# Kernel tuning notes

Measured on AMD Instinct MI355X. Metric: run time of the kernel, lower is better.

The kernel has to match this reference:

```python
import jax, jax.numpy as jnp
import numpy as np

DIM = 8          # per-head dim
ATT_EPS = 1e-15  # LiteMLA eps
BN_EPS = 1e-5    # torch BatchNorm2d default eps


def conv2d(x, w, groups=1, pad=0):
    # x: NCHW, w: OIHW
    return jax.lax.conv_general_dilated(
        x, w, window_strides=(1, 1), padding=[(pad, pad), (pad, pad)],
        dimension_numbers=('NCHW', 'OIHW', 'NCHW'), feature_group_count=groups)


def setup_inputs() -> dict:
    key = jax.random.key(0)
    ks = jax.random.split(key, 6)
    B, C, H, W = 4, 128, 128, 128
    heads = C // DIM            # 16
    t3 = 3 * C                  # 3*total_dim = 384
    x = jax.random.normal(ks[0], (B, C, H, W), jnp.float32)
    w_qkv = jax.random.normal(ks[1], (t3, C, 1, 1), jnp.float32) * 0.02
    w_dw = jax.random.normal(ks[2], (t3, 1, 5, 5), jnp.float32) * 0.02      # depthwise 5x5
    w_pw = jax.random.normal(ks[3], (t3, t3 // (3 * heads), 1, 1), jnp.float32) * 0.05  # grouped 1x1, groups=3*heads
    w_proj = jax.random.normal(ks[4], (C, 2 * C, 1, 1), jnp.float32) * 0.02  # proj 1x1: 2C -> C
    bn_gamma = jnp.ones((C,), jnp.float32)
    bn_beta = jnp.zeros((C,), jnp.float32)
    bn_mean = jnp.zeros((C,), jnp.float32)
    bn_var = jnp.ones((C,), jnp.float32)
    return dict(x=x, w_qkv=w_qkv, w_dw=w_dw, w_pw=w_pw, w_proj=w_proj,
                bn_gamma=bn_gamma, bn_beta=bn_beta, bn_mean=bn_mean, bn_var=bn_var)


def reference(x, w_qkv, w_dw, w_pw, w_proj, bn_gamma, bn_beta, bn_mean, bn_var):
    # qkv: 1x1 conv, no norm / no act
    qkv = conv2d(x, w_qkv)                                  # (B, 3C, H, W)
    t3 = w_qkv.shape[0]
    # aggreg[0]: depthwise 5x5 + grouped 1x1
    groups_pw = t3 // w_pw.shape[1]                         # 3*heads
    agg = conv2d(conv2d(qkv, w_dw, groups=t3, pad=2), w_pw, groups=groups_pw)
    qkv = jnp.concatenate([qkv, agg], axis=1)               # (B, 6C, H, W)

    B, _, H, W = qkv.shape
    N = H * W
    qkv = qkv.reshape(B, -1, 3 * DIM, N)                    # (B, 2*heads, 3*dim, N)
    q = jax.nn.relu(qkv[:, :, :DIM])                        # (B, h, d, N)
    k = jax.nn.relu(qkv[:, :, DIM:2 * DIM])                 # (B, h, d, N)
    v = qkv[:, :, 2 * DIM:]                                 # (B, h, d, N)
    # pad v with a row of ones for normalization
    v = jnp.concatenate([v, jnp.ones_like(v[:, :, :1])], axis=2)  # (B, h, d+1, N)

    vk = jnp.einsum('bhdn,bhen->bhde', v, k)                # (B, h, d+1, d)
    out = jnp.einsum('bhde,bhen->bhdn', vk, q)              # (B, h, d+1, N)
    out = out[:, :, :-1] / (out[:, :, -1:] + ATT_EPS)       # (B, h, d, N)
    out = out.reshape(B, -1, H, W)                          # (B, 2C, H, W)

    # proj: 1x1 conv + BatchNorm2d (inference), no act
    out = conv2d(out, w_proj)                               # (B, C, H, W)
    inv = bn_gamma / jnp.sqrt(bn_var + BN_EPS)
    out = out * inv[:, None, None] + (bn_beta - bn_mean * inv)[:, None, None]
    return out
```

## Files before the change

### kernel.cpp

```cpp
#include <hip/hip_runtime.h>

#define BB 4
#define CIN 128
#define T3 384
#define HH 128
#define WW 128
#define NPIX 16384
#define QKV_ELE (BB*T3*NPIX)

#define SEC 4160
#define KGP 1040
#define PLN 520

typedef __attribute__((ext_vector_type(8))) short bf16x8;
typedef __attribute__((ext_vector_type(4))) float f32x4;

__device__ __forceinline__ unsigned splitpack(float x) {
  unsigned u = __float_as_uint(x);
  unsigned hb = (u + 0x7fffu + ((u >> 16) & 1u)) >> 16;
  float lo = x - __uint_as_float(hb << 16);
  unsigned ul = __float_as_uint(lo);
  unsigned lb = (ul + 0x7fffu + ((ul >> 16) & 1u)) >> 16;
  return (hb << 16) | (lb & 0xffffu);
}

__device__ __forceinline__ void packpair(float a, float b, unsigned& hi, unsigned& lo) {
  unsigned p0 = splitpack(a), p1 = splitpack(b);
  hi = (p1 & 0xffff0000u) | (p0 >> 16);
  lo = (p1 << 16) | (p0 & 0xffffu);
}

__global__ __launch_bounds__(256) void k0_wprep(const float* __restrict__ wqkv,
                                                unsigned* __restrict__ wimg,
                                                float* __restrict__ zbuf) {
  int id = blockIdx.x * 256 + threadIdx.x;
  if (id < 16) zbuf[id] = 0.f;
  int i = id & 3;
  int co = (id >> 2) & 127;
  int kgrp = (id >> 9) & 3;
  int c = (id >> 11) & 3;
  int m = id >> 13;
  int ci = c * 32 + kgrp * 8 + 2 * i;
  const float* wrow = wqkv + (size_t)(m * 128 + co) * 128 + ci;
  unsigned hi, lo;
  packpair(wrow[0], wrow[1], hi, lo);
  size_t base = (size_t)(m * 4 + c) * SEC + kgrp * KGP + co * 4 + i;
  wimg[base] = hi;
  wimg[base + PLN] = lo;
}

__global__ __launch_bounds__(256) void k1_qkv_mfma(const float* __restrict__ x,
                                                   const unsigned* __restrict__ wimg,
                                                   float* __restrict__ qkv) {
  __shared__ __align__(16) unsigned Xp[4 * KGP];
  __shared__ __align__(16) unsigned Wp[4 * KGP];
  const int t = threadIdx.x;
  const int p = blockIdx.x;
  const int qd = p / 24;
  const int r_ = p - qd * 24;
  const int m = r_ >> 3;
  const int tt = qd * 8 + (r_ & 7);
  const int n0 = (tt & 127) * 128;
  const int b = tt >> 7;
  const float* xb = x + (size_t)b * CIN * NPIX + n0;

  const int l = t & 63;
  const int w = t >> 6;
  const int g = l >> 4;
  const int lc = l & 15;
  const int ch = w >> 1;
  const int nh = w & 1;
  const int kg = t >> 6;
  const int nn_ = t & 63;

  f32x4 acc[4][4];
  #pragma unroll
  for (int i = 0; i < 4; ++i)
    #pragma unroll
    for (int j = 0; j < 4; ++j) acc[i][j] = (f32x4){0.f, 0.f, 0.f, 0.f};

  for (int c = 0; c < 4; ++c) {
    {
      const uint4* wsrc = (const uint4*)(wimg + (size_t)(m * 4 + c) * SEC);
      uint4* wdst = (uint4*)Wp;
      #pragma unroll
      for (int r = 0; r < 5; ++r) {
        int idx = t + r * 256;
        if (idx < 1040) wdst[idx] = wsrc[idx];
      }
    }
    {
      const float* colbase = xb + (size_t)(c * 32 + kg * 8) * NPIX;
      #pragma unroll
      for (int half = 0; half < 2; ++half) {
        int n = nn_ + half * 64;
        const float* colp = colbase + n;
        unsigned hp[4], lp[4];
        #pragma unroll
        for (int i = 0; i < 4; ++i)
          packpair(colp[(size_t)(2 * i) * NPIX], colp[(size_t)(2 * i + 1) * NPIX],
                   hp[i], lp[i]);
        *(uint4*)&Xp[kg * KGP + n * 4] = make_uint4(hp[0], hp[1], hp[2], hp[3]);
        *(uint4*)&Xp[kg * KGP + PLN + n * 4] = make_uint4(lp[0], lp[1], lp[2], lp[3]);
      }
    }
    __syncthreads();

    bf16x8 bh[4], bl[4];
    #pragma unroll
    for (int ng = 0; ng < 4; ++ng) {
      const int nb = (nh * 64 + ng * 16 + lc) * 4;
      bh[ng] = *(const bf16x8*)&Xp[g * KGP + nb];
      bl[ng] = *(const bf16x8*)&Xp[g * KGP + PLN + nb];
    }
    #pragma unroll
    for (int cg = 0; cg < 4; ++cg) {
      const int cb = (ch * 64 + cg * 16 + lc) * 4;
      bf16x8 ah = *(const bf16x8*)&Wp[g * KGP + cb];
      bf16x8 al = *(const bf16x8*)&Wp[g * KGP + PLN + cb];
      #pragma unroll
      for (int ng = 0; ng < 4; ++ng) {
        acc[cg][ng] = __builtin_amdgcn_mfma_f32_16x16x32_bf16(ah, bh[ng], acc[cg][ng], 0, 0, 0);
        acc[cg][ng] = __builtin_amdgcn_mfma_f32_16x16x32_bf16(ah, bl[ng], acc[cg][ng], 0, 0, 0);
        acc[cg][ng] = __builtin_amdgcn_mfma_f32_16x16x32_bf16(al, bh[ng], acc[cg][ng], 0, 0, 0);
      }
    }
    __syncthreads();
  }
  #pragma unroll
  for (int cg = 0; cg < 4; ++cg) {
    const size_t corow = (size_t)b * T3 + m * 128 + ch * 64 + cg * 16 + g * 4;
    #pragma unroll
    for (int ng = 0; ng < 4; ++ng) {
      const int nn = n0 + nh * 64 + ng * 16 + lc;
      #pragma unroll
      for (int rr = 0; rr < 4; ++rr)
        qkv[(corow + rr) * NPIX + nn] = acc[cg][ng][rr];
    }
  }
}

#define PDW 36

__device__ __forceinline__ void dw_compute(const float* __restrict__ plane,
                                           const float* __restrict__ w25,
                                           const float* __restrict__ zbuf,
                                           int x0, int y0, int xq, int yg,
                                           float dacc[4][4]) {
  const int gx0 = x0 + 4 * xq - 4;
  const bool ex0 = (gx0 >= 0);
  const bool ex2 = (gx0 + 11 < WW);
  f32x4 u[8][3];
  #pragma unroll
  for (int r = 0; r < 8; ++r) {
    const int gy = y0 + 4 * yg - 2 + r;
    const bool iny = (unsigned)gy < (unsigned)HH;
    const float* rp = plane + gy * WW + gx0;
    const float* p0 = (iny && ex0) ? rp : zbuf;
    const float* p1 = iny ? (rp + 4) : zbuf;
    const float* p2 = (iny && ex2) ? (rp + 8) : zbuf;
    u[r][0] = *(const f32x4*)p0;
    u[r][1] = *(const f32x4*)p1;
    u[r][2] = *(const f32x4*)p2;
  }
  #pragma unroll
  for (int jy = 0; jy < 4; ++jy)
    #pragma unroll
    for (int jx = 0; jx < 4; ++jx) dacc[jy][jx] = 0.f;
  #pragma unroll
  for (int r = 0; r < 8; ++r) {
    float vals[12] = {u[r][0][0], u[r][0][1], u[r][0][2], u[r][0][3],
                      u[r][1][0], u[r][1][1], u[r][1][2], u[r][1][3],
                      u[r][2][0], u[r][2][1], u[r][2][2], u[r][2][3]};
    #pragma unroll
    for (int jy = 0; jy < 4; ++jy) {
      int ky = r - jy;
      if (ky < 0 || ky > 4) continue;
      #pragma unroll
      for (int kx = 0; kx < 5; ++kx) {
        float wv = w25[ky * 5 + kx];
        #pragma unroll
        for (int jx = 0; jx < 4; ++jx)
          dacc[jy][jx] += wv * vals[jx + kx + 2];
      }
    }
  }
}

__device__ __forceinline__ void vk_reduce(const float* __restrict__ kb,
                                          const float* __restrict__ vb,
                                          float* __restrict__ pr, int t) {
  const int wv = t >> 6;
  const int lane = t & 63;
  const int d0 = wv * 2;
  float accA[8], accB[8], accS[8];
  #pragma unroll
  for (int e = 0; e < 8; ++e) { accA[e] = 0.f; accB[e] = 0.f; accS[e] = 0.f; }
  #pragma unroll
  for (int it = 0; it < 8; ++it) {
    int p = it * 64 + lane;
    float kv[8];
    #pragma unroll
    for (int e = 0; e < 8; ++e) kv[e] = kb[e * 512 + p];
    float vA = vb[d0 * 512 + p];
    float vB = vb[(d0 + 1) * 512 + p];
    #pragma unroll
    for (int e = 0; e < 8; ++e) { accA[e] += vA * kv[e]; accB[e] += vB * kv[e]; }
    if (wv == 0) {
      #pragma unroll
      for (int e = 0; e < 8; ++e) accS[e] += kv[e];
    }
  }
  #pragma unroll
  for (int e = 0; e < 8; ++e) {
    #pragma unroll
    for (int m = 1; m < 64; m <<= 1) {
      accA[e] += __shfl_xor(accA[e], m);
      accB[e] += __shfl_xor(accB[e], m);
    }
  }
  if (wv == 0) {
    #pragma unroll
    for (int e = 0; e < 8; ++e)
      #pragma unroll
      for (int m = 1; m < 64; m <<= 1) accS[e] += __shfl_xor(accS[e], m);
  }
  if (lane == 0) {
    #pragma unroll
    for (int e = 0; e < 8; ++e) {
      pr[d0 * 8 + e] = accA[e];
      pr[(d0 + 1) * 8 + e] = accB[e];
    }
    if (wv == 0) {
      #pragma unroll
      for (int e = 0; e < 8; ++e) pr[64 + e] = accS[e];
    }
  }
}

__global__ __launch_bounds__(256, 4) void k2_fused(const float* __restrict__ qkv,
                                                   const float* __restrict__ wdw,
                                                   const float* __restrict__ wpw,
                                                   const float* __restrict__ zbuf,
                                                   float* __restrict__ agg,
                                                   float* __restrict__ part2) {
  __shared__ __align__(16) float bufA[8 * 16 * PDW];
  __shared__ __align__(16) float bufB[8 * 16 * PDW];
  __shared__ float wds[24][25];
  __shared__ float wps[192];
  const int t = threadIdx.x;
  const int p = blockIdx.x;
  const int L = (p & 7) * 256 + (p >> 3);
  const int z = L >> 5;
  const int rem = L & 31;
  const int x0 = (rem & 3) * 32;
  const int y0 = (rem >> 2) * 16;
  const int b = z >> 4;
  const int hh = z & 15;
  const float* src = qkv + ((size_t)b * T3 + hh * 24) * NPIX;

  for (int idx = t; idx < 600; idx += 256)
    wds[idx / 25][idx % 25] = wdw[(size_t)hh * 600 + idx];
  if (t < 192) wps[t] = wpw[hh * 192 + t];
  __syncthreads();

  const int ch = t >> 5;
  const int xq = t & 7;
  const int yg = (t >> 3) & 3;

  {
    float daccK[4][4], daccV[4][4];
    dw_compute(src + (size_t)(8 + ch) * NPIX, &wds[8 + ch][0], zbuf, x0, y0, xq, yg, daccK);
    dw_compute(src + (size_t)(16 + ch) * NPIX, &wds[16 + ch][0], zbuf, x0, y0, xq, yg, daccV);
    #pragma unroll
    for (int jy = 0; jy < 4; ++jy) {
      *(float4*)&bufA[ch * (16 * PDW) + (yg * 4 + jy) * PDW + xq * 4] =
          make_float4(daccK[jy][0], daccK[jy][1], daccK[jy][2], daccK[jy][3]);
      *(float4*)&bufB[ch * (16 * PDW) + (yg * 4 + jy) * PDW + xq * 4] =
          make_float4(daccV[jy][0], daccV[jy][1], daccV[jy][2], daccV[jy][3]);
    }
  }
  __syncthreads();

  float kout[2][8], vout[2][8];
  #pragma unroll
  for (int pp = 0; pp < 2; ++pp) {
    int pix = t + pp * 256;
    int py = pix >> 5, px = pix & 31;
    float dvA[8], dvB[8];
    #pragma unroll
    for (int ic = 0; ic < 8; ++ic) {
      dvA[ic] = bufA[ic * (16 * PDW) + py * PDW + px];
      dvB[ic] = bufB[ic * (16 * PDW) + py * PDW + px];
    }
    #pragma unroll
    for (int oc = 0; oc < 8; ++oc) {
      float sk = 0.f, sv = 0.f;
      #pragma unroll
      for (int ic = 0; ic < 8; ++ic) {
        sk += wps[64 + oc * 8 + ic] * dvA[ic];
        sv += wps[128 + oc * 8 + ic] * dvB[ic];
      }
      kout[pp][oc] = sk;
      vout[pp][oc] = sv;
    }
  }
  __syncthreads();

  #pragma unroll
  for (int pp = 0; pp < 2; ++pp) {
    int pix = t + pp * 256;
    #pragma unroll
    for (int oc = 0; oc < 8; ++oc) {
      bufA[oc * 512 + pix] = fmaxf(kout[pp][oc], 0.f);
      bufB[oc * 512 + pix] = vout[pp][oc];
    }
  }
  __syncthreads();

  f32x4 rs[8];
  #pragma unroll
  for (int j = 0; j < 8; ++j) {
    int qd2 = t + j * 256;
    int buf = qd2 >> 10;
    int ch2 = (qd2 >> 7) & 7;
    int r2 = qd2 & 127;
    int py = r2 >> 3, qx = r2 & 7;
    const float* gp = src + (size_t)(8 + buf * 8 + ch2) * NPIX + (y0 + py) * WW + x0 + qx * 4;
    rs[j] = *(const f32x4*)gp;
  }
  vk_reduce(bufA, bufB, part2 + ((size_t)(z * 2 + 1) * 32 + rem) * 72, t);
  __syncthreads();

  #pragma unroll
  for (int j = 0; j < 8; ++j) {
    int qd2 = t + j * 256;
    int buf = qd2 >> 10;
    int ch2 = (qd2 >> 7) & 7;
    int r2 = qd2 & 127;
    int py = r2 >> 3, qx = r2 & 7;
    f32x4 v = rs[j];
    if (buf == 0) {
      v[0] = fmaxf(v[0], 0.f); v[1] = fmaxf(v[1], 0.f);
      v[2] = fmaxf(v[2], 0.f); v[3] = fmaxf(v[3], 0.f);
      *(f32x4*)&bufA[ch2 * 512 + py * 32 + qx * 4] = v;
    } else {
      *(f32x4*)&bufB[ch2 * 512 + py * 32 + qx * 4] = v;
    }
  }
  __syncthreads();

  vk_reduce(bufA, bufB, part2 + ((size_t)(z * 2 + 0) * 32 + rem) * 72, t);
  __syncthreads();

  {
    float dacc[4][4];
    dw_compute(src + (size_t)ch * NPIX, &wds[ch][0], zbuf, x0, y0, xq, yg, dacc);
    #pragma unroll
    for (int jy = 0; jy < 4; ++jy)
      *(float4*)&bufA[ch * (16 * PDW) + (yg * 4 + jy) * PDW + xq * 4] =
          make_float4(dacc[jy][0], dacc[jy][1], dacc[jy][2], dacc[jy][3]);
  }
  __syncthreads();
  float* dst = agg + ((size_t)b * T3 + hh * 24) * NPIX + (size_t)y0 * WW + x0;
  #pragma unroll
  for (int pp = 0; pp < 2; ++pp) {
    int pix = t + pp * 256;
    int py = pix >> 5, px = pix & 31;
    float dv[8];
    #pragma unroll
    for (int ic = 0; ic < 8; ++ic) dv[ic] = bufA[ic * (16 * PDW) + py * PDW + px];
    #pragma unroll
    for (int oc = 0; oc < 8; ++oc) {
      float s = 0.f;
      #pragma unroll
      for (int ic = 0; ic < 8; ++ic) s += wps[oc * 8 + ic] * dv[ic];
      dst[(size_t)oc * NPIX + py * WW + px] = s;
    }
  }
}

__global__ __launch_bounds__(128) void k3b_sum(const float* __restrict__ part2,
                                               float* __restrict__ vk) {
  const int bh = blockIdx.x;
  const int j = threadIdx.x;
  if (j < 72) {
    int b = bh >> 5, h = bh & 31;
    int z = b * 16 + (h & 15);
    int ph = h >> 4;
    const float* srcp = part2 + ((size_t)(z * 2 + ph) * 32) * 72 + j;
    float s = 0.f;
    #pragma unroll
    for (int c = 0; c < 32; ++c) s += srcp[(size_t)c * 72];
    vk[(size_t)bh * 72 + j] = s;
  }
}

__global__ __launch_bounds__(256) void k3c_M(const float* __restrict__ wproj,
                                             const float* __restrict__ vk,
                                             const float* __restrict__ gamma,
                                             const float* __restrict__ beta,
                                             const float* __restrict__ mean,
                                             const float* __restrict__ var,
                                             unsigned* __restrict__ Mimg,
                                             float* __restrict__ shiftb) {
  int id = blockIdx.x * 256 + threadIdx.x;
  int i = id & 3;
  int co = (id >> 2) & 127;
  int kgrp = (id >> 9) & 3;
  int cidx = (id >> 11) & 7;
  int b = id >> 14;
  int h = cidx * 4 + kgrp;
  float inv = gamma[co] * rsqrtf(var[co] + 1e-5f);
  const float* wrow = wproj + (size_t)co * 256 + h * 8;
  const float* vkc = vk + ((size_t)b * 32 + h) * 72;
  float s0 = 0.f, s1 = 0.f;
  #pragma unroll
  for (int d = 0; d < 8; ++d) {
    float wv = wrow[d];
    s0 += wv * vkc[d * 8 + 2 * i];
    s1 += wv * vkc[d * 8 + 2 * i + 1];
  }
  unsigned hi, lo;
  packpair(inv * s0, inv * s1, hi, lo);
  size_t base = (size_t)(b * 8 + cidx) * SEC + kgrp * KGP + co * 4 + i;
  Mimg[base] = hi;
  Mimg[base + PLN] = lo;
  if (b == 0 && cidx == 0 && kgrp == 0 && i == 0)
    shiftb[co] = beta[co] - mean[co] * inv;
}

__global__ __launch_bounds__(256) void k4_mfma(const float* __restrict__ qkv,
                                               const float* __restrict__ agg,
                                               const float* __restrict__ vk,
                                               const unsigned* __restrict__ Mimg,
                                               const float* __restrict__ shiftb,
                                               float* __restrict__ out) {
  __shared__ __align__(16) unsigned Ap[4 * KGP];
  __shared__ __align__(16) unsigned Bp[4 * KGP];
  const int t = threadIdx.x;
  const int n0 = blockIdx.x * 128;
  const int b = blockIdx.y;

  const int l = t & 63;
  const int w = t >> 6;
  const int g = l >> 4;
  const int lc = l & 15;
  const int ch = w >> 1;
  const int nh = w & 1;
  const int hj = t >> 6;
  const int nn_ = t & 63;

  f32x4 acc[4][4];
  #pragma unroll
  for (int i = 0; i < 4; ++i)
    #pragma unroll
    for (int j = 0; j < 4; ++j) acc[i][j] = (f32x4){0.f, 0.f, 0.f, 0.f};

  for (int cidx = 0; cidx < 8; ++cidx) {
    {
      const uint4* asrc = (const uint4*)(Mimg + (size_t)(b * 8 + cidx) * SEC);
      uint4* adst = (uint4*)Ap;
      #pragma unroll
      for (int r = 0; r < 5; ++r) {
        int idx = t + r * 256;
        if (idx < 1040) adst[idx] = asrc[idx];
      }
    }
    {
      const int h = cidx * 4 + hj;
      const float* srcb = (h < 16 ? qkv : agg) +
                          ((size_t)b * T3 + (h & 15) * 24) * NPIX + n0;
      const float* vkr = vk + ((size_t)b * 32 + h) * 72 + 64;
      float vv[8];
      #pragma unroll
      for (int e = 0; e < 8; ++e) vv[e] = vkr[e];
      #pragma unroll
      for (int half = 0; half < 2; ++half) {
        int n = nn_ + half * 64;
        float q[8];
        float den = 1e-15f;
        #pragma unroll
        for (int e = 0; e < 8; ++e) {
          q[e] = fmaxf(srcb[(size_t)e * NPIX + n], 0.f);
          den += vv[e] * q[e];
        }
        float rd = 1.0f / den;
        unsigned hp[4], lp[4];
        #pragma unroll
        for (int i = 0; i < 4; ++i)
          packpair(q[2 * i] * rd, q[2 * i + 1] * rd, hp[i], lp[i]);
        *(uint4*)&Bp[hj * KGP + n * 4] = make_uint4(hp[0], hp[1], hp[2], hp[3]);
        *(uint4*)&Bp[hj * KGP + PLN + n * 4] = make_uint4(lp[0], lp[1], lp[2], lp[3]);
      }
    }
    __syncthreads();

    bf16x8 bh[4], bl[4];
    #pragma unroll
    for (int ng = 0; ng < 4; ++ng) {
      const int nb = (nh * 64 + ng * 16 + lc) * 4;
      bh[ng] = *(const bf16x8*)&Bp[g * KGP + nb];
      bl[ng] = *(const bf16x8*)&Bp[g * KGP + PLN + nb];
    }
    #pragma unroll
    for (int cg = 0; cg < 4; ++cg) {
      const int cb = (ch * 64 + cg * 16 + lc) * 4;
      bf16x8 ah = *(const bf16x8*)&Ap[g * KGP + cb];
      bf16x8 al = *(const bf16x8*)&Ap[g * KGP + PLN + cb];
      #pragma unroll
      for (int ng = 0; ng < 4; ++ng) {
        acc[cg][ng] = __builtin_amdgcn_mfma_f32_16x16x32_bf16(ah, bh[ng], acc[cg][ng], 0, 0, 0);
        acc[cg][ng] = __builtin_amdgcn_mfma_f32_16x16x32_bf16(ah, bl[ng], acc[cg][ng], 0, 0, 0);
        acc[cg][ng] = __builtin_amdgcn_mfma_f32_16x16x32_bf16(al, bh[ng], acc[cg][ng], 0, 0, 0);
      }
    }
    __syncthreads();
  }
  #pragma unroll
  for (int cg = 0; cg < 4; ++cg) {
    const int cobase = ch * 64 + cg * 16 + g * 4;
    #pragma unroll
    for (int ng = 0; ng < 4; ++ng) {
      const int nn = n0 + nh * 64 + ng * 16 + lc;
      #pragma unroll
      for (int rr = 0; rr < 4; ++rr) {
        int co = cobase + rr;
        out[((size_t)b * 128 + co) * NPIX + nn] = acc[cg][ng][rr] + shiftb[co];
      }
    }
  }
}

__global__ void fill_sentinel(float* o, int n) {
  int i = blockIdx.x * 256 + threadIdx.x;
  if (i < n) o[i] = 12345.0f;
}

extern "C" void kernel_launch(void* const* d_in, const int* in_sizes, int n_in,
                              void* d_out, int out_size, void* d_ws, size_t ws_size,
                              hipStream_t stream) {
  const float* x     = (const float*)d_in[0];
  const float* wqkv  = (const float*)d_in[1];
  const float* wdw   = (const float*)d_in[2];
  const float* wpw   = (const float*)d_in[3];
  const float* wproj = (const float*)d_in[4];
  const float* gamma = (const float*)d_in[5];
  const float* beta  = (const float*)d_in[6];
  const float* mean  = (const float*)d_in[7];
  const float* var   = (const float*)d_in[8];
  float* out = (float*)d_out;
  float* ws = (float*)d_ws;

  const size_t part2F = 64 * 2 * 32 * 72;
  const size_t mimgF = 32 * SEC;
  const size_t wimgF = 12 * SEC;
  const size_t needF = (size_t)QKV_ELE * 2 + part2F + 9216 + 128 + mimgF + wimgF + 16;
  if (ws_size < needF * 4) {
    fill_sentinel<<<dim3((out_size + 255) / 256), dim3(256), 0, stream>>>(out, out_size);
    return;
  }
  float* qkv    = ws;
  float* agg    = qkv + QKV_ELE;
  float* part2  = agg + QKV_ELE;
  float* vkbuf  = part2 + part2F;
  float* shiftb = vkbuf + 9216;
  unsigned* Mimg = (unsigned*)(shiftb + 128);
  unsigned* wimg = Mimg + mimgF;
  float* zbuf   = (float*)(wimg + wimgF);

  k0_wprep<<<dim3(96), 256, 0, stream>>>(wqkv, wimg, zbuf);
  k1_qkv_mfma<<<dim3(1536), 256, 0, stream>>>(x, wimg, qkv);
  k2_fused<<<dim3(2048), 256, 0, stream>>>(qkv, wdw, wpw, zbuf, agg, part2);
  k3b_sum<<<dim3(128), 128, 0, stream>>>(part2, vkbuf);
  k3c_M<<<dim3(256), 256, 0, stream>>>(wproj, vkbuf, gamma, beta, mean, var, Mimg, shiftb);
  k4_mfma<<<dim3(128, 4), 256, 0, stream>>>(qkv, agg, vkbuf, Mimg, shiftb, out);
}
```

Baseline: 160.3 us.

## Split fused depthwise kernel into Q and KV kernels, halve k4 pixel tile

The fused k2 kernel is split in two. k2_q computes the Q-branch depthwise and grouped conv into agg. k2_kv computes the K/V branches with the V loads issued early to overlap the K pointwise stage, then does the vk reductions. Separately, k4 now covers 64 pixels per block instead of 128, doubling its grid to raise occupancy and parallelism. The cost is an extra launch, re-reading of the qkv planes and A-operand loads across more blocks, and higher LDS use in k2_kv.

```diff
diff --git a/kernel.cpp b/kernel.cpp
--- a/kernel.cpp
+++ b/kernel.cpp
@@ -11,6 +11,8 @@
 #define SEC 4160
 #define KGP 1040
 #define PLN 520
+#define KGPB 520
+#define PLNB 260
 
 typedef __attribute__((ext_vector_type(8))) short bf16x8;
 typedef __attribute__((ext_vector_type(4))) float f32x4;
@@ -142,15 +144,13 @@
 
 #define PDW 36
 
-__device__ __forceinline__ void dw_compute(const float* __restrict__ plane,
-                                           const float* __restrict__ w25,
-                                           const float* __restrict__ zbuf,
-                                           int x0, int y0, int xq, int yg,
-                                           float dacc[4][4]) {
+__device__ __forceinline__ void dw_load(const float* __restrict__ plane,
+                                        const float* __restrict__ zbuf,
+                                        int x0, int y0, int xq, int yg,
+                                        f32x4 u[8][3]) {
   const int gx0 = x0 + 4 * xq - 4;
   const bool ex0 = (gx0 >= 0);
   const bool ex2 = (gx0 + 11 < WW);
-  f32x4 u[8][3];
   #pragma unroll
   for (int r = 0; r < 8; ++r) {
     const int gy = y0 + 4 * yg - 2 + r;
@@ -163,6 +163,11 @@
     u[r][1] = *(const f32x4*)p1;
     u[r][2] = *(const f32x4*)p2;
   }
+}
+
+__device__ __forceinline__ void dw_math(const f32x4 u[8][3],
+                                        const float* __restrict__ w25,
+                                        float dacc[4][4]) {
   #pragma unroll
   for (int jy = 0; jy < 4; ++jy)
     #pragma unroll
@@ -187,67 +192,14 @@
   }
 }
 
-__device__ __forceinline__ void vk_reduce(const float* __restrict__ kb,
-                                          const float* __restrict__ vb,
-                                          float* __restrict__ pr, int t) {
-  const int wv = t >> 6;
-  const int lane = t & 63;
-  const int d0 = wv * 2;
-  float accA[8], accB[8], accS[8];
-  #pragma unroll
-  for (int e = 0; e < 8; ++e) { accA[e] = 0.f; accB[e] = 0.f; accS[e] = 0.f; }
-  #pragma unroll
-  for (int it = 0; it < 8; ++it) {
-    int p = it * 64 + lane;
-    float kv[8];
-    #pragma unroll
-    for (int e = 0; e < 8; ++e) kv[e] = kb[e * 512 + p];
-    float vA = vb[d0 * 512 + p];
-    float vB = vb[(d0 + 1) * 512 + p];
-    #pragma unroll
-    for (int e = 0; e < 8; ++e) { accA[e] += vA * kv[e]; accB[e] += vB * kv[e]; }
-    if (wv == 0) {
-      #pragma unroll
-      for (int e = 0; e < 8; ++e) accS[e] += kv[e];
-    }
-  }
-  #pragma unroll
-  for (int e = 0; e < 8; ++e) {
-    #pragma unroll
-    for (int m = 1; m < 64; m <<= 1) {
-      accA[e] += __shfl_xor(accA[e], m);
-      accB[e] += __shfl_xor(accB[e], m);
-    }
-  }
-  if (wv == 0) {
-    #pragma unroll
-    for (int e = 0; e < 8; ++e)
-      #pragma unroll
-      for (int m = 1; m < 64; m <<= 1) accS[e] += __shfl_xor(accS[e], m);
-  }
-  if (lane == 0) {
-    #pragma unroll
-    for (int e = 0; e < 8; ++e) {
-      pr[d0 * 8 + e] = accA[e];
-      pr[(d0 + 1) * 8 + e] = accB[e];
-    }
-    if (wv == 0) {
-      #pragma unroll
-      for (int e = 0; e < 8; ++e) pr[64 + e] = accS[e];
-    }
-  }
-}
-
-__global__ __launch_bounds__(256, 4) void k2_fused(const float* __restrict__ qkv,
-                                                   const float* __restrict__ wdw,
-                                                   const float* __restrict__ wpw,
-                                                   const float* __restrict__ zbuf,
-                                                   float* __restrict__ agg,
-                                                   float* __restrict__ part2) {
-  __shared__ __align__(16) float bufA[8 * 16 * PDW];
-  __shared__ __align__(16) float bufB[8 * 16 * PDW];
-  __shared__ float wds[24][25];
-  __shared__ float wps[192];
+__global__ __launch_bounds__(256, 2) void k2_q(const float* __restrict__ qkv,
+                                               const float* __restrict__ wdw,
+                                               const float* __restrict__ wpw,
+                                               const float* __restrict__ zbuf,
+                                               float* __restrict__ agg) {
+  __shared__ __align__(16) float dws[8 * 16 * PDW];
+  __shared__ float wds[8][25];
+  __shared__ float wps[64];
   const int t = threadIdx.x;
   const int p = blockIdx.x;
   const int L = (p & 7) * 256 + (p >> 3);
@@ -259,61 +211,181 @@
   const int hh = z & 15;
   const float* src = qkv + ((size_t)b * T3 + hh * 24) * NPIX;
 
-  for (int idx = t; idx < 600; idx += 256)
+  for (int idx = t; idx < 200; idx += 256)
     wds[idx / 25][idx % 25] = wdw[(size_t)hh * 600 + idx];
-  if (t < 192) wps[t] = wpw[hh * 192 + t];
+  if (t < 64) wps[t] = wpw[hh * 192 + t];
   __syncthreads();
 
   const int ch = t >> 5;
   const int xq = t & 7;
   const int yg = (t >> 3) & 3;
 
+  f32x4 u[8][3];
+  dw_load(src + (size_t)ch * NPIX, zbuf, x0, y0, xq, yg, u);
+  float dacc[4][4];
+  dw_math(u, &wds[ch][0], dacc);
+
+  #pragma unroll
+  for (int jy = 0; jy < 4; ++jy) {
+    float4 o = make_float4(dacc[jy][0], dacc[jy][1], dacc[jy][2], dacc[jy][3]);
+    *(float4*)&dws[ch * (16 * PDW) + (yg * 4 + jy) * PDW + xq * 4] = o;
+  }
+  __syncthreads();
+
+  float* dst = agg + ((size_t)b * T3 + hh * 24) * NPIX + (size_t)y0 * WW + x0;
+  #pragma unroll
+  for (int pp = 0; pp < 2; ++pp) {
+    int pix = t + pp * 256;
+    int py = pix >> 5;
+    int px = pix & 31;
+    float dv[8];
+    #pragma unroll
+    for (int ic = 0; ic < 8; ++ic) dv[ic] = dws[ic * (16 * PDW) + py * PDW + px];
+    #pragma unroll
+    for (int oc = 0; oc < 8; ++oc) {
+      float s = 0.f;
+      #pragma unroll
+      for (int ic = 0; ic < 8; ++ic) s += wps[oc * 8 + ic] * dv[ic];
+      dst[(size_t)oc * NPIX + py * WW + px] = s;
+    }
+  }
+}
+
+__device__ __forceinline__ void vk_reduce(const float* __restrict__ kb,
+                                          const float* __restrict__ vb,
+                                          float* __restrict__ pr, int t) {
+  const int wv = t >> 6;
+  const int lane = t & 63;
+  const int d0 = wv * 2;
+  float accA[8], accB[8], accS[8];
+  #pragma unroll
+  for (int e = 0; e < 8; ++e) { accA[e] = 0.f; accB[e] = 0.f; accS[e] = 0.f; }
+  #pragma unroll
+  for (int it = 0; it < 8; ++it) {
+    int p = it * 64 + lane;
+    float kv[8];
+    #pragma unroll
+    for (int e = 0; e < 8; ++e) kv[e] = kb[e * 512 + p];
+    float vA = vb[d0 * 512 + p];
+    float vB = vb[(d0 + 1) * 512 + p];
+    #pragma unroll
+    for (int e = 0; e < 8; ++e) { accA[e] += vA * kv[e]; accB[e] += vB * kv[e]; }
+    if (wv == 0) {
+      #pragma unroll
+      for (int e = 0; e < 8; ++e) accS[e] += kv[e];
+    }
+  }
+  #pragma unroll
+  for (int e = 0; e < 8; ++e) {
+    #pragma unroll
+    for (int m = 1; m < 64; m <<= 1) {
+      accA[e] += __shfl_xor(accA[e], m);
+      accB[e] += __shfl_xor(accB[e], m);
+    }
+  }
+  if (wv == 0) {
+    #pragma unroll
+    for (int e = 0; e < 8; ++e)
+      #pragma unroll
+      for (int m = 1; m < 64; m <<= 1) accS[e] += __shfl_xor(accS[e], m);
+  }
+  if (lane == 0) {
+    #pragma unroll
+    for (int e = 0; e < 8; ++e) {
+      pr[d0 * 8 + e] = accA[e];
+      pr[(d0 + 1) * 8 + e] = accB[e];
+    }
+    if (wv == 0) {
+      #pragma unroll
+      for (int e = 0; e < 8; ++e) pr[64 + e] = accS[e];
+    }
+  }
+}
+
+__global__ __launch_bounds__(256, 2) void k2_kv(const float* __restrict__ qkv,
+                                                const float* __restrict__ wdw,
+                                                const float* __restrict__ wpw,
+                                                const float* __restrict__ zbuf,
+                                                float* __restrict__ part2) {
+  __shared__ __align__(16) float buf1[8 * 16 * PDW];
+  __shared__ __align__(16) float kbuf[8 * 512];
+  __shared__ __align__(16) float vbuf[8 * 512];
+  __shared__ float wds[16][25];
+  __shared__ float wps[128];
+  const int t = threadIdx.x;
+  const int p = blockIdx.x;
+  const int L = (p & 7) * 256 + (p >> 3);
+  const int z = L >> 5;
+  const int rem = L & 31;
+  const int x0 = (rem & 3) * 32;
+  const int y0 = (rem >> 2) * 16;
+  const int b = z >> 4;
+  const int hh = z & 15;
+  const float* src = qkv + ((size_t)b * T3 + hh * 24) * NPIX;
+
+  for (int idx = t; idx < 400; idx += 256)
+    wds[idx / 25][idx % 25] = wdw[(size_t)hh * 600 + 200 + idx];
+  if (t < 128) wps[t] = wpw[hh * 192 + 64 + t];
+  __syncthreads();
+
+  const int ch = t >> 5;
+  const int xq = t & 7;
+  const int yg = (t >> 3) & 3;
+
   {
-    float daccK[4][4], daccV[4][4];
-    dw_compute(src + (size_t)(8 + ch) * NPIX, &wds[8 + ch][0], zbuf, x0, y0, xq, yg, daccK);
-    dw_compute(src + (size_t)(16 + ch) * NPIX, &wds[16 + ch][0], zbuf, x0, y0, xq, yg, daccV);
-    #pragma unroll
-    for (int jy = 0; jy < 4; ++jy) {
-      *(float4*)&bufA[ch * (16 * PDW) + (yg * 4 + jy) * PDW + xq * 4] =
-          make_float4(daccK[jy][0], daccK[jy][1], daccK[jy][2], daccK[jy][3]);
-      *(float4*)&bufB[ch * (16 * PDW) + (yg * 4 + jy) * PDW + xq * 4] =
-          make_float4(daccV[jy][0], daccV[jy][1], daccV[jy][2], daccV[jy][3]);
-    }
-  }
-  __syncthreads();
-
-  float kout[2][8], vout[2][8];
+    f32x4 uK[8][3];
+    dw_load(src + (size_t)(8 + ch) * NPIX, zbuf, x0, y0, xq, yg, uK);
+    float dacc[4][4];
+    dw_math(uK, &wds[ch][0], dacc);
+    #pragma unroll
+    for (int jy = 0; jy < 4; ++jy)
+      *(float4*)&buf1[ch * (16 * PDW) + (yg * 4 + jy) * PDW + xq * 4] =
+          make_float4(dacc[jy][0], dacc[jy][1], dacc[jy][2], dacc[jy][3]);
+  }
+  __syncthreads();
+
+  f32x4 uV[8][3];
+  dw_load(src + (size_t)(16 + ch) * NPIX, zbuf, x0, y0, xq, yg, uV);
   #pragma unroll
   for (int pp = 0; pp < 2; ++pp) {
     int pix = t + pp * 256;
     int py = pix >> 5, px = pix & 31;
-    float dvA[8], dvB[8];
-    #pragma unroll
-    for (int ic = 0; ic < 8; ++ic) {
-      dvA[ic] = bufA[ic * (16 * PDW) + py * PDW + px];
-      dvB[ic] = bufB[ic * (16 * PDW) + py * PDW + px];
-    }
+    float dv[8];
+    #pragma unroll
+    for (int ic = 0; ic < 8; ++ic) dv[ic] = buf1[ic * (16 * PDW) + py * PDW + px];
     #pragma unroll
     for (int oc = 0; oc < 8; ++oc) {
-      float sk = 0.f, sv = 0.f;
-      #pragma unroll
-      for (int ic = 0; ic < 8; ++ic) {
-        sk += wps[64 + oc * 8 + ic] * dvA[ic];
-        sv += wps[128 + oc * 8 + ic] * dvB[ic];
-      }
-      kout[pp][oc] = sk;
-      vout[pp][oc] = sv;
-    }
+      float s = 0.f;
+      #pragma unroll
+      for (int ic = 0; ic < 8; ++ic) s += wps[oc * 8 + ic] * dv[ic];
+      kbuf[oc * 512 + pix] = fmaxf(s, 0.f);
+    }
+  }
+  __syncthreads();
+
+  {
+    float dacc[4][4];
+    dw_math(uV, &wds[8 + ch][0], dacc);
+    #pragma unroll
+    for (int jy = 0; jy < 4; ++jy)
+      *(float4*)&buf1[ch * (16 * PDW) + (yg * 4 + jy) * PDW + xq * 4] =
+          make_float4(dacc[jy][0], dacc[jy][1], dacc[jy][2], dacc[jy][3]);
   }
   __syncthreads();
 
   #pragma unroll
   for (int pp = 0; pp < 2; ++pp) {
     int pix = t + pp * 256;
+    int py = pix >> 5, px = pix & 31;
+    float dv[8];
+    #pragma unroll
+    for (int ic = 0; ic < 8; ++ic) dv[ic] = buf1[ic * (16 * PDW) + py * PDW + px];
     #pragma unroll
     for (int oc = 0; oc < 8; ++oc) {
-      bufA[oc * 512 + pix] = fmaxf(kout[pp][oc], 0.f);
-      bufB[oc * 512 + pix] = vout[pp][oc];
+      float s = 0.f;
+      #pragma unroll
+      for (int ic = 0; ic < 8; ++ic) s += wps[64 + oc * 8 + ic] * dv[ic];
+      vbuf[oc * 512 + pix] = s;
     }
   }
   __syncthreads();
@@ -329,7 +401,7 @@
     const float* gp = src + (size_t)(8 + buf * 8 + ch2) * NPIX + (y0 + py) * WW + x0 + qx * 4;
     rs[j] = *(const f32x4*)gp;
   }
-  vk_reduce(bufA, bufB, part2 + ((size_t)(z * 2 + 1) * 32 + rem) * 72, t);
+  vk_reduce(kbuf, vbuf, part2 + ((size_t)(z * 2 + 1) * 32 + rem) * 72, t);
   __syncthreads();
 
   #pragma unroll
@@ -343,41 +415,14 @@
     if (buf == 0) {
       v[0] = fmaxf(v[0], 0.f); v[1] = fmaxf(v[1], 0.f);
       v[2] = fmaxf(v[2], 0.f); v[3] = fmaxf(v[3], 0.f);
-      *(f32x4*)&bufA[ch2 * 512 + py * 32 + qx * 4] = v;
+      *(f32x4*)&kbuf[ch2 * 512 + py * 32 + qx * 4] = v;
     } else {
-      *(f32x4*)&bufB[ch2 * 512 + py * 32 + qx * 4] = v;
-    }
-  }
-  __syncthreads();
-
-  vk_reduce(bufA, bufB, part2 + ((size_t)(z * 2 + 0) * 32 + rem) * 72, t);
-  __syncthreads();
-
-  {
-    float dacc[4][4];
-    dw_compute(src + (size_t)ch * NPIX, &wds[ch][0], zbuf, x0, y0, xq, yg, dacc);
-    #pragma unroll
-    for (int jy = 0; jy < 4; ++jy)
-      *(float4*)&bufA[ch * (16 * PDW) + (yg * 4 + jy) * PDW + xq * 4] =
-          make_float4(dacc[jy][0], dacc[jy][1], dacc[jy][2], dacc[jy][3]);
-  }
-  __syncthreads();
-  float* dst = agg + ((size_t)b * T3 + hh * 24) * NPIX + (size_t)y0 * WW + x0;
-  #pragma unroll
-  for (int pp = 0; pp < 2; ++pp) {
-    int pix = t + pp * 256;
-    int py = pix >> 5, px = pix & 31;
-    float dv[8];
-    #pragma unroll
-    for (int ic = 0; ic < 8; ++ic) dv[ic] = bufA[ic * (16 * PDW) + py * PDW + px];
-    #pragma unroll
-    for (int oc = 0; oc < 8; ++oc) {
-      float s = 0.f;
-      #pragma unroll
-      for (int ic = 0; ic < 8; ++ic) s += wps[oc * 8 + ic] * dv[ic];
-      dst[(size_t)oc * NPIX + py * WW + px] = s;
-    }
-  }
+      *(f32x4*)&vbuf[ch2 * 512 + py * 32 + qx * 4] = v;
+    }
+  }
+  __syncthreads();
+
+  vk_reduce(kbuf, vbuf, part2 + ((size_t)(z * 2 + 0) * 32 + rem) * 72, t);
 }
 
 __global__ __launch_bounds__(128) void k3b_sum(const float* __restrict__ part2,
@@ -437,9 +482,9 @@
                                                const float* __restrict__ shiftb,
                                                float* __restrict__ out) {
   __shared__ __align__(16) unsigned Ap[4 * KGP];
-  __shared__ __align__(16) unsigned Bp[4 * KGP];
+  __shared__ __align__(16) unsigned Bp[4 * KGPB];
   const int t = threadIdx.x;
-  const int n0 = blockIdx.x * 128;
+  const int n0 = blockIdx.x * 64;
   const int b = blockIdx.y;
 
   const int l = t & 63;
@@ -451,11 +496,11 @@
   const int hj = t >> 6;
   const int nn_ = t & 63;
 
-  f32x4 acc[4][4];
+  f32x4 acc[4][2];
   #pragma unroll
   for (int i = 0; i < 4; ++i)
     #pragma unroll
-    for (int j = 0; j < 4; ++j) acc[i][j] = (f32x4){0.f, 0.f, 0.f, 0.f};
+    for (int j = 0; j < 2; ++j) acc[i][j] = (f32x4){0.f, 0.f, 0.f, 0.f};
 
   for (int cidx = 0; cidx < 8; ++cidx) {
     {
@@ -470,38 +515,31 @@
     {
       const int h = cidx * 4 + hj;
       const float* srcb = (h < 16 ? qkv : agg) +
-                          ((size_t)b * T3 + (h & 15) * 24) * NPIX + n0;
+                          ((size_t)b * T3 + (h & 15) * 24) * NPIX + n0 + nn_;
       const float* vkr = vk + ((size_t)b * 32 + h) * 72 + 64;
-      float vv[8];
-      #pragma unroll
-      for (int e = 0; e < 8; ++e) vv[e] = vkr[e];
-      #pragma unroll
-      for (int half = 0; half < 2; ++half) {
-        int n = nn_ + half * 64;
-        float q[8];
-        float den = 1e-15f;
-        #pragma unroll
-        for (int e = 0; e < 8; ++e) {
-          q[e] = fmaxf(srcb[(size_t)e * NPIX + n], 0.f);
-          den += vv[e] * q[e];
-        }
-        float rd = 1.0f / den;
-        unsigned hp[4], lp[4];
-        #pragma unroll
-        for (int i = 0; i < 4; ++i)
-          packpair(q[2 * i] * rd, q[2 * i + 1] * rd, hp[i], lp[i]);
-        *(uint4*)&Bp[hj * KGP + n * 4] = make_uint4(hp[0], hp[1], hp[2], hp[3]);
-        *(uint4*)&Bp[hj * KGP + PLN + n * 4] = make_uint4(lp[0], lp[1], lp[2], lp[3]);
-      }
+      float q[8];
+      float den = 1e-15f;
+      #pragma unroll
+      for (int e = 0; e < 8; ++e) {
+        q[e] = fmaxf(srcb[(size_t)e * NPIX], 0.f);
+        den += vkr[e] * q[e];
+      }
+      float rd = 1.0f / den;
+      unsigned hp[4], lp[4];
+      #pragma unroll
+      for (int i = 0; i < 4; ++i)
+        packpair(q[2 * i] * rd, q[2 * i + 1] * rd, hp[i], lp[i]);
+      *(uint4*)&Bp[hj * KGPB + nn_ * 4] = make_uint4(hp[0], hp[1], hp[2], hp[3]);
+      *(uint4*)&Bp[hj * KGPB + PLNB + nn_ * 4] = make_uint4(lp[0], lp[1], lp[2], lp[3]);
     }
     __syncthreads();
 
-    bf16x8 bh[4], bl[4];
-    #pragma unroll
-    for (int ng = 0; ng < 4; ++ng) {
-      const int nb = (nh * 64 + ng * 16 + lc) * 4;
-      bh[ng] = *(const bf16x8*)&Bp[g * KGP + nb];
-      bl[ng] = *(const bf16x8*)&Bp[g * KGP + PLN + nb];
+    bf16x8 bhf[2], blf[2];
+    #pragma unroll
+    for (int ng = 0; ng < 2; ++ng) {
+      const int nb = (nh * 32 + ng * 16 + lc) * 4;
+      bhf[ng] = *(const bf16x8*)&Bp[g * KGPB + nb];
+      blf[ng] = *(const bf16x8*)&Bp[g * KGPB + PLNB + nb];
     }
     #pragma unroll
     for (int cg = 0; cg < 4; ++cg) {
@@ -509,10 +547,10 @@
       bf16x8 ah = *(const bf16x8*)&Ap[g * KGP + cb];
       bf16x8 al = *(const bf16x8*)&Ap[g * KGP + PLN + cb];
       #pragma unroll
-      for (int ng = 0; ng < 4; ++ng) {
-        acc[cg][ng] = __builtin_amdgcn_mfma_f32_16x16x32_bf16(ah, bh[ng], acc[cg][ng], 0, 0, 0);
-        acc[cg][ng] = __builtin_amdgcn_mfma_f32_16x16x32_bf16(ah, bl[ng], acc[cg][ng], 0, 0, 0);
-        acc[cg][ng] = __builtin_amdgcn_mfma_f32_16x16x32_bf16(al, bh[ng], acc[cg][ng], 0, 0, 0);
+      for (int ng = 0; ng < 2; ++ng) {
+        acc[cg][ng] = __builtin_amdgcn_mfma_f32_16x16x32_bf16(ah, bhf[ng], acc[cg][ng], 0, 0, 0);
+        acc[cg][ng] = __builtin_amdgcn_mfma_f32_16x16x32_bf16(ah, blf[ng], acc[cg][ng], 0, 0, 0);
+        acc[cg][ng] = __builtin_amdgcn_mfma_f32_16x16x32_bf16(al, bhf[ng], acc[cg][ng], 0, 0, 0);
       }
     }
     __syncthreads();
@@ -521,8 +559,8 @@
   for (int cg = 0; cg < 4; ++cg) {
     const int cobase = ch * 64 + cg * 16 + g * 4;
     #pragma unroll
-    for (int ng = 0; ng < 4; ++ng) {
-      const int nn = n0 + nh * 64 + ng * 16 + lc;
+    for (int ng = 0; ng < 2; ++ng) {
+      const int nn = n0 + nh * 32 + ng * 16 + lc;
       #pragma unroll
       for (int rr = 0; rr < 4; ++rr) {
         int co = cobase + rr;
@@ -571,8 +609,9 @@
 
   k0_wprep<<<dim3(96), 256, 0, stream>>>(wqkv, wimg, zbuf);
   k1_qkv_mfma<<<dim3(1536), 256, 0, stream>>>(x, wimg, qkv);
-  k2_fused<<<dim3(2048), 256, 0, stream>>>(qkv, wdw, wpw, zbuf, agg, part2);
+  k2_q<<<dim3(2048), 256, 0, stream>>>(qkv, wdw, wpw, zbuf, agg);
+  k2_kv<<<dim3(2048), 256, 0, stream>>>(qkv, wdw, wpw, zbuf, part2);
   k3b_sum<<<dim3(128), 128, 0, stream>>>(part2, vkbuf);
   k3c_M<<<dim3(256), 256, 0, stream>>>(wproj, vkbuf, gamma, beta, mean, var, Mimg, shiftb);
-  k4_mfma<<<dim3(128, 4), 256, 0, stream>>>(qkv, agg, vkbuf, Mimg, shiftb, out);
-}
+  k4_mfma<<<dim3(256, 4), 256, 0, stream>>>(qkv, agg, vkbuf, Mimg, shiftb, out);
+}
```

New measurement: 154.2 us. -3.8%, faster.
